# Optimization experiments

Measured on AMD Instinct MI355X. Metric: run time of the kernel, lower is better.

Reference implementation:

```python
import jax, jax.numpy as jnp
import numpy as np

P = 8192      # num_pois
U = 4096      # num_users
E = 4096      # num directed hyperedges
D = 128       # emb_dim
B = 1024      # batch of user indices
T_UP = 1.0    # args.t1
T_GEO = 1.0   # args.t2
T_P2P = 1.0   # args.t3
ALPHA = 0.8   # constant alpha in Geo_ODEFunc


def setup_inputs() -> dict:
    key = jax.random.key(0)
    ks = jax.random.split(key, 13)
    return {
        "poi_emb_weight": jax.random.normal(ks[0], (P + 1, D), jnp.float32) * 0.02,
        "w_gate_geo": jax.random.normal(ks[1], (D, D), jnp.float32) * 0.05,
        "b_gate_geo": jax.random.normal(ks[2], (1, D), jnp.float32) * 0.05,
        "w_gate_seq": jax.random.normal(ks[3], (D, D), jnp.float32) * 0.05,
        "b_gate_seq": jax.random.normal(ks[4], (1, D), jnp.float32) * 0.05,
        "w_gate_col": jax.random.normal(ks[5], (D, D), jnp.float32) * 0.05,
        "b_gate_col": jax.random.normal(ks[6], (1, D), jnp.float32) * 0.05,
        "HG_up": jax.random.uniform(ks[7], (U, P), jnp.float32) * (1.0 / P),
        "HG_pu": jax.random.uniform(ks[8], (P, U), jnp.float32) * (1.0 / U),
        "HG_poi_src": jax.random.uniform(ks[9], (P, E), jnp.float32) * (1.0 / E),
        "HG_poi_tar": jax.random.uniform(ks[10], (E, P), jnp.float32) * (1.0 / P),
        "poi_geo_graph": jax.random.uniform(ks[11], (P, P), jnp.float32) * (1.0 / P),
        "user_idx": jax.random.randint(ks[12], (B,), 0, U, jnp.int32),
    }


def _gate(pe, w, b):
    # pois_embs * sigmoid(pois_embs @ W + b)
    return pe * jax.nn.sigmoid(pe @ w + b)


def reference(poi_emb_weight, w_gate_geo, b_gate_geo, w_gate_seq, b_gate_seq,
              w_gate_col, b_gate_col, HG_up, HG_pu, HG_poi_src, HG_poi_tar,
              poi_geo_graph, user_idx):
    pe = poi_emb_weight[:-1]                      # drop padding row -> [P, D]
    geo_gate = _gate(pe, w_gate_geo, b_gate_geo)
    seq_gate = _gate(pe, w_gate_seq, b_gate_seq)
    col_gate = _gate(pe, w_gate_col, b_gate_col)

    # U2P ODE, single Euler step on t=[0, T_UP]:
    #   f(x) = (HG_pu@HG_up - I)@x + e, e = x0; A@x factored to avoid [P,P].
    x = col_gate
    hg_pois = x + T_UP * (HG_pu @ (HG_up @ x) - x + x)

    # Geo ODE: f(x) = (alpha/2)*G@x - x + e, e = x0, alpha = 0.8.
    g = geo_gate
    geo_pois = g + T_GEO * ((ALPHA / 2.0) * (poi_geo_graph @ g) - g + g)

    # P2P (directed hypergraph) ODE: A = src@tar, f(x) = (A - I)@x + e.
    s = seq_gate
    trans_pois = s + T_P2P * (HG_poi_src @ (HG_poi_tar @ s) - s + s)

    # structural user embeddings, gathered at batch indices
    hg_users = (HG_up @ hg_pois)[user_idx]        # [B, D]
    geo_users = (HG_up @ geo_pois)[user_idx]      # [B, D]

    # [3P + 2B, D]
    return jnp.concatenate([hg_pois, geo_pois, trans_pois, hg_users, geo_users], axis=0)
```

## Files before the change

kernel.cpp:

```cpp
#include <hip/hip_runtime.h>
#include <hip/hip_bf16.h>

#define PP 8192
#define UU 4096
#define EE 4096
#define BB 1024

using f32x4  = __attribute__((ext_vector_type(4))) float;
using u32x4  = __attribute__((ext_vector_type(4))) unsigned int;
using bf16x8 = __attribute__((ext_vector_type(8))) short;
typedef __hip_bfloat16 bf16_t;

__device__ __forceinline__ unsigned cvt2(float a, float b){
  unsigned r;
  asm("v_cvt_pk_bf16_f32 %0, %1, %2" : "=v"(r) : "v"(a), "v"(b));
  return r;
}

__device__ __forceinline__ void gload16(const void* g, void* l){
  __builtin_amdgcn_global_load_lds((const __attribute__((address_space(1))) void*)g,
                                   (__attribute__((address_space(3))) void*)l, 16, 0, 0);
}

struct Job {
  const float*  A;
  const bf16_t* Bt;
  const float*  add;
  const float*  bvec;
  float*        outF;
  bf16_t*       outT;
  int           outTstride;
  float         scale;
  int           K;
  int           nb;
  int           mode;
};

#define ABUF 32768
#define BBUF 16384
#define BOFF 65536

__global__ __launch_bounds__(256, 1) void gemm_big(Job j0, Job j1, Job j2){
  __shared__ char smem[2*ABUF + 3*BBUF];
  int bid = blockIdx.x;
  Job j = j0;
  if (bid >= j.nb){ bid -= j.nb; j = j1; if (bid >= j.nb){ bid -= j.nb; j = j2; } }
  const int K  = j.K;
  const int S  = K >> 8;
  const int T4 = K >> 6;
  const int m0 = bid << 5;
  const int tid = threadIdx.x;
  const int lane = tid & 63;
  const int wid = tid >> 6;
  const int wm = wid >> 1, wk = wid & 1;
  const int s0 = bid & (S - 1);

  const char* Ab = (const char*)j.A;
  const char* Bb = (const char*)j.Bt;

  size_t a_srcb[8]; unsigned a_ldsb[8];
  #pragma unroll
  for (int i = 0; i < 8; ++i){
    int r = wid*8 + i;
    a_srcb[i] = (size_t)(m0 + r)*(size_t)K*4 + (size_t)((unsigned)(lane*16) ^ ((r & 15) << 4));
    a_ldsb[i] = (unsigned)(r * 1024);
  }
  size_t b_srcb[4]; unsigned b_ldsb[4];
  #pragma unroll
  for (int i = 0; i < 4; ++i){
    int L = wid*4 + i;
    int n = L*8 + (lane>>3);
    b_srcb[i] = (size_t)n*(size_t)K*2 + (size_t)(((lane & 7) << 4) ^ ((n & 7) << 4));
    b_ldsb[i] = (unsigned)(BOFF + L * 1024);
  }

  const int arow = wm*16 + (lane & 15);
  const unsigned aswz = (unsigned)((arow & 15) << 4);
  const unsigned kbase = (unsigned)(wk*128 + ((lane>>4) << 5));
  const unsigned ard = (unsigned)(arow*1024) + (kbase ^ aswz);
  unsigned b_rd[8];
  #pragma unroll
  for (int n0 = 0; n0 < 8; ++n0){
    int n = n0*16 + (lane & 15);
    unsigned c = (unsigned)(wk*64 + ((lane>>4) << 4));
    b_rd[n0] = (unsigned)(BOFF + n*128) + (c ^ ((n & 7) << 4));
  }

  const f32x4 fzero = {0.f, 0.f, 0.f, 0.f};
  f32x4 acc[8];
  #pragma unroll
  for (int i = 0; i < 8; ++i) acc[i] = fzero;

  auto STAGE_A = [&](int s){
    char* l = smem + (unsigned)(s & 1) * ABUF;
    size_t ka = (size_t)((unsigned)(s + s0) & (unsigned)(S - 1)) * 1024;
    #pragma unroll
    for (int i = 0; i < 8; ++i) gload16(Ab + a_srcb[i] + ka, l + a_ldsb[i]);
  };
  auto STAGE_B = [&](int lstep){
    char* l = smem + (unsigned)(lstep % 3) * BBUF;
    size_t kb = (size_t)((unsigned)(lstep + 4*s0) & (unsigned)(T4 - 1)) * 128;
    #pragma unroll
    for (int i = 0; i < 4; ++i) gload16(Bb + b_srcb[i] + kb, l + b_ldsb[i]);
  };
  auto COMP = [&](unsigned aoff, unsigned boff){
    unsigned aa = aoff + ard;
    f32x4 a0, a1;
    asm volatile("ds_read_b128 %0, %2\n\tds_read_b128 %1, %3"
                 : "=&v"(a0), "=&v"(a1) : "v"(aa), "v"(aa ^ 16u));
    bf16x8 b0,b1,b2,b3,b4,b5,b6,b7;
    asm volatile("ds_read_b128 %0, %1" : "=v"(b0) : "v"(boff + b_rd[0]));
    asm volatile("ds_read_b128 %0, %1" : "=v"(b1) : "v"(boff + b_rd[1]));
    asm volatile("ds_read_b128 %0, %1" : "=v"(b2) : "v"(boff + b_rd[2]));
    asm volatile("ds_read_b128 %0, %1" : "=v"(b3) : "v"(boff + b_rd[3]));
    asm volatile("ds_read_b128 %0, %1" : "=v"(b4) : "v"(boff + b_rd[4]));
    asm volatile("ds_read_b128 %0, %1" : "=v"(b5) : "v"(boff + b_rd[5]));
    asm volatile("ds_read_b128 %0, %1" : "=v"(b6) : "v"(boff + b_rd[6]));
    asm volatile("ds_read_b128 %0, %1" : "=v"(b7) : "v"(boff + b_rd[7]));
    asm volatile("s_waitcnt lgkmcnt(0)" ::: "memory");
    __builtin_amdgcn_sched_barrier(0);
    union { bf16x8 v; unsigned u[4]; } af;
    af.u[0] = cvt2(a0.x, a0.y);
    af.u[1] = cvt2(a0.z, a0.w);
    af.u[2] = cvt2(a1.x, a1.y);
    af.u[3] = cvt2(a1.z, a1.w);
    acc[0] = __builtin_amdgcn_mfma_f32_16x16x32_bf16(af.v, b0, acc[0], 0,0,0);
    acc[1] = __builtin_amdgcn_mfma_f32_16x16x32_bf16(af.v, b1, acc[1], 0,0,0);
    acc[2] = __builtin_amdgcn_mfma_f32_16x16x32_bf16(af.v, b2, acc[2], 0,0,0);
    acc[3] = __builtin_amdgcn_mfma_f32_16x16x32_bf16(af.v, b3, acc[3], 0,0,0);
    acc[4] = __builtin_amdgcn_mfma_f32_16x16x32_bf16(af.v, b4, acc[4], 0,0,0);
    acc[5] = __builtin_amdgcn_mfma_f32_16x16x32_bf16(af.v, b5, acc[5], 0,0,0);
    acc[6] = __builtin_amdgcn_mfma_f32_16x16x32_bf16(af.v, b6, acc[6], 0,0,0);
    acc[7] = __builtin_amdgcn_mfma_f32_16x16x32_bf16(af.v, b7, acc[7], 0,0,0);
  };

  #define WAITV(n) asm volatile("s_waitcnt vmcnt(" #n ")" ::: "memory")
  #define BAR __builtin_amdgcn_s_barrier()

  STAGE_A(0); STAGE_B(0); STAGE_B(1);

  for (int s = 0; s < S - 1; ++s){
    const unsigned ao = (unsigned)(s & 1) * ABUF;
    const int l = 4*s;
    STAGE_A(s + 1); STAGE_B(l + 2);
    WAITV(16); BAR; COMP(ao + 0*256, (unsigned)((l+0) % 3) * BBUF); BAR;
    STAGE_B(l + 3);
    WAITV(16); BAR; COMP(ao + 1*256, (unsigned)((l+1) % 3) * BBUF); BAR;
    STAGE_B(l + 4);
    WAITV(8);  BAR; COMP(ao + 2*256, (unsigned)((l+2) % 3) * BBUF); BAR;
    STAGE_B(l + 5);
    WAITV(8);  BAR; COMP(ao + 3*256, (unsigned)((l+3) % 3) * BBUF); BAR;
  }
  {
    const int s = S - 1;
    const unsigned ao = (unsigned)(s & 1) * ABUF;
    const int l = 4*s;
    STAGE_B(l + 2);
    WAITV(8); BAR; COMP(ao + 0*256, (unsigned)((l+0) % 3) * BBUF); BAR;
    STAGE_B(l + 3);
    WAITV(8); BAR; COMP(ao + 1*256, (unsigned)((l+1) % 3) * BBUF); BAR;
    WAITV(4); BAR; COMP(ao + 2*256, (unsigned)((l+2) % 3) * BBUF); BAR;
    WAITV(0); BAR; COMP(ao + 3*256, (unsigned)((l+3) % 3) * BBUF); BAR;
  }

  __syncthreads();
  float* red = (float*)smem;
  if (wk == 1){
    #pragma unroll
    for (int n0 = 0; n0 < 8; ++n0)
      #pragma unroll
      for (int q = 0; q < 4; ++q){
        int row = wm*16 + ((lane>>4)<<2) + q;
        int col = n0*16 + (lane & 15);
        red[row*128 + col] = acc[n0][q];
      }
  }
  __syncthreads();
  if (wk == 0){
    #pragma unroll
    for (int n0 = 0; n0 < 8; ++n0)
      #pragma unroll
      for (int q = 0; q < 4; ++q){
        int row = wm*16 + ((lane>>4)<<2) + q;
        int col = n0*16 + (lane & 15);
        float v = (acc[n0][q] + red[row*128 + col]) * j.scale;
        size_t gp = (size_t)(m0 + row);
        if (j.mode == 1){
          float pe = j.add[gp*128 + col];
          float bb = j.bvec[col];
          v = pe / (1.f + __expf(-(v + bb)));
        } else if (j.add){
          v += j.add[gp*128 + col];
        }
        acc[n0][q] = v;
        if (j.outF) j.outF[gp*128 + col] = v;
      }
  }

  if (j.outT){
    __syncthreads();
    if (wk == 0){
      #pragma unroll
      for (int n0 = 0; n0 < 8; ++n0)
        #pragma unroll
        for (int q = 0; q < 4; ++q){
          int row = wm*16 + ((lane>>4)<<2) + q;
          int col = n0*16 + (lane & 15);
          red[row*128 + col] = acc[n0][q];
        }
    }
    __syncthreads();
    int col = tid & 127, seg = tid >> 7;
    unsigned wrds[8] __attribute__((aligned(16)));
    #pragma unroll
    for (int r = 0; r < 8; ++r){
      float v0 = red[(seg*16 + 2*r    )*128 + col];
      float v1 = red[(seg*16 + 2*r + 1)*128 + col];
      wrds[r] = cvt2(v0, v1);
    }
    bf16_t* dst = j.outT + (size_t)col * (size_t)j.outTstride + (m0 + seg*16);
    *(u32x4*)dst       = *(const u32x4*)&wrds[0];
    *((u32x4*)dst + 1) = *(const u32x4*)&wrds[4];
  }
}

#define GTBUF 24576

__global__ __launch_bounds__(256, 2) void gemm_gates(Job j0, Job j1, Job j2){
  __shared__ char smem[3*GTBUF];
  int bid = blockIdx.x;
  Job j = j0;
  if (bid >= j.nb){ bid -= j.nb; j = j1; if (bid >= j.nb){ bid -= j.nb; j = j2; } }
  const int K = j.K;
  const int T = K >> 6;
  const int m0 = bid << 5;
  const int tid = threadIdx.x;
  const int lane = tid & 63;
  const int wid = tid >> 6;
  const int wm = wid >> 1, wk = wid & 1;

  const char* Ab = (const char*)j.A;
  const char* Bb = (const char*)j.Bt;

  size_t a_src[2]; unsigned a_lds[2];
  #pragma unroll
  for (int i = 0; i < 2; ++i){
    int row = wid*8 + i*4 + (lane>>4);
    unsigned sb = (lane & 15) << 4;
    a_src[i] = (size_t)(m0 + row)*(size_t)K*4 + (size_t)(sb ^ ((row & 15) << 4));
    a_lds[i] = (unsigned)((wid*8 + i*4) * 256);
  }
  size_t b_src[4]; unsigned b_lds[4];
  #pragma unroll
  for (int i = 0; i < 4; ++i){
    int n  = wid*32 + i*8 + (lane>>3);
    unsigned sb = (lane & 7) << 4;
    b_src[i] = (size_t)n*(size_t)K*2 + (size_t)(sb ^ ((n & 7) << 4));
    b_lds[i] = (unsigned)(8192 + (wid*32 + i*8) * 128);
  }

  const int arow = wm*16 + (lane & 15);
  const unsigned acb  = (unsigned)(wk*128 + ((lane>>4) * 32));
  const unsigned aswz = (unsigned)((arow & 15) << 4);
  const unsigned a_rd0 = arow*256 + (acb ^ aswz);
  const unsigned a_rd1 = arow*256 + ((acb + 16) ^ aswz);
  unsigned b_rd[8];
  #pragma unroll
  for (int n0 = 0; n0 < 8; ++n0){
    int n = n0*16 + (lane & 15);
    unsigned c = (unsigned)(wk*64 + ((lane>>4) * 16));
    b_rd[n0] = 8192u + n*128 + (c ^ ((n & 7) << 4));
  }

  const f32x4 fzero = {0.f, 0.f, 0.f, 0.f};
  f32x4 acc[8];
  #pragma unroll
  for (int i = 0; i < 8; ++i) acc[i] = fzero;

  auto STAGE = [&](unsigned bufoff, int t){
    char* l = smem + bufoff;
    size_t ka = (size_t)t * 256;
    size_t kb = (size_t)t * 128;
    #pragma unroll
    for (int i = 0; i < 2; ++i) gload16(Ab + a_src[i] + ka, l + a_lds[i]);
    #pragma unroll
    for (int i = 0; i < 4; ++i) gload16(Bb + b_src[i] + kb, l + b_lds[i]);
  };

  STAGE(0, 0);
  if (T > 1){
    STAGE(GTBUF, 1);
    asm volatile("s_waitcnt vmcnt(6)" ::: "memory");
  } else {
    asm volatile("s_waitcnt vmcnt(0)" ::: "memory");
  }
  __builtin_amdgcn_s_barrier();

  for (int t = 0; t < T; ++t){
    char* l = smem + (unsigned)(t % 3) * GTBUF;
    if (t + 2 < T) STAGE((unsigned)((t+2) % 3) * GTBUF, t + 2);
    f32x4 a0 = *(const f32x4*)(l + a_rd0);
    f32x4 a1 = *(const f32x4*)(l + a_rd1);
    union { bf16x8 v; unsigned u[4]; } af;
    af.u[0] = cvt2(a0.x, a0.y);
    af.u[1] = cvt2(a0.z, a0.w);
    af.u[2] = cvt2(a1.x, a1.y);
    af.u[3] = cvt2(a1.z, a1.w);
    #pragma unroll
    for (int n0 = 0; n0 < 8; ++n0){
      bf16x8 bfr = *(const bf16x8*)(l + b_rd[n0]);
      acc[n0] = __builtin_amdgcn_mfma_f32_16x16x32_bf16(af.v, bfr, acc[n0], 0, 0, 0);
    }
    if (t + 1 < T){
      if (t + 2 < T) asm volatile("s_waitcnt vmcnt(6)" ::: "memory");
      else           asm volatile("s_waitcnt vmcnt(0)" ::: "memory");
      __builtin_amdgcn_s_barrier();
    }
  }

  __syncthreads();
  float* red = (float*)smem;
  if (wk == 1){
    #pragma unroll
    for (int n0 = 0; n0 < 8; ++n0)
      #pragma unroll
      for (int q = 0; q < 4; ++q){
        int row = wm*16 + ((lane>>4)<<2) + q;
        int col = n0*16 + (lane & 15);
        red[row*128 + col] = acc[n0][q];
      }
  }
  __syncthreads();
  if (wk == 0){
    #pragma unroll
    for (int n0 = 0; n0 < 8; ++n0)
      #pragma unroll
      for (int q = 0; q < 4; ++q){
        int row = wm*16 + ((lane>>4)<<2) + q;
        int col = n0*16 + (lane & 15);
        float v = (acc[n0][q] + red[row*128 + col]) * j.scale;
        size_t gp = (size_t)(m0 + row);
        if (j.mode == 1){
          float pe = j.add[gp*128 + col];
          float bb = j.bvec[col];
          v = pe / (1.f + __expf(-(v + bb)));
        } else if (j.add){
          v += j.add[gp*128 + col];
        }
        acc[n0][q] = v;
        if (j.outF) j.outF[gp*128 + col] = v;
      }
  }

  if (j.outT){
    __syncthreads();
    if (wk == 0){
      #pragma unroll
      for (int n0 = 0; n0 < 8; ++n0)
        #pragma unroll
        for (int q = 0; q < 4; ++q){
          int row = wm*16 + ((lane>>4)<<2) + q;
          int col = n0*16 + (lane & 15);
          red[row*128 + col] = acc[n0][q];
        }
    }
    __syncthreads();
    int col = tid & 127, seg = tid >> 7;
    unsigned wrds[8] __attribute__((aligned(16)));
    #pragma unroll
    for (int r = 0; r < 8; ++r){
      float v0 = red[(seg*16 + 2*r    )*128 + col];
      float v1 = red[(seg*16 + 2*r + 1)*128 + col];
      wrds[r] = cvt2(v0, v1);
    }
    bf16_t* dst = j.outT + (size_t)col * (size_t)j.outTstride + (m0 + seg*16);
    *(u32x4*)dst       = *(const u32x4*)&wrds[0];
    *((u32x4*)dst + 1) = *(const u32x4*)&wrds[4];
  }
}

#define GBUFB 40960

__global__ __launch_bounds__(256, 1) void gemm_gather(const float* __restrict__ Aup,
    const int* __restrict__ uidx, const bf16_t* __restrict__ B5t, float* __restrict__ partials){
  __shared__ char smem[3*GBUFB];
  const int bid = blockIdx.x;
  const int mtile = bid & 31, split = bid >> 5;
  const int tid = threadIdx.x, lane = tid & 63, wid = tid >> 6;
  const int wm = wid >> 1, wk = wid & 1;
  const int T = 16;
  const char* Ab = (const char*)Aup;
  const char* Bb = (const char*)B5t;

  size_t a_src[2]; unsigned a_lds[2];
  #pragma unroll
  for (int i = 0; i < 2; ++i){
    int row  = wid*8 + i*4 + (lane>>4);
    int grow = uidx[mtile*32 + row];
    unsigned sb = (lane & 15) << 4;
    a_src[i] = (size_t)grow*(size_t)(PP*4) + (size_t)((sb ^ ((row & 15) << 4)) + split*4096);
    a_lds[i] = (unsigned)((wid*8 + i*4) * 256);
  }
  size_t b_src[8]; unsigned b_lds[8];
  #pragma unroll
  for (int i = 0; i < 8; ++i){
    int n  = wid*64 + i*8 + (lane>>3);
    unsigned sb = (lane & 7) << 4;
    b_src[i] = (size_t)n*(size_t)(PP*2) + (size_t)((sb ^ ((n & 7) << 4)) + split*2048);
    b_lds[i] = (unsigned)(8192 + (wid*64 + i*8) * 128);
  }
  const int arow = wm*16 + (lane & 15);
  const unsigned acb  = (unsigned)(wk*128 + ((lane>>4)*32));
  const unsigned aswz = (unsigned)((arow & 15) << 4);
  const unsigned a_rd0 = arow*256 + (acb ^ aswz);
  const unsigned a_rd1 = arow*256 + ((acb + 16) ^ aswz);
  unsigned b_rd[16];
  #pragma unroll
  for (int n0 = 0; n0 < 16; ++n0){
    int n = n0*16 + (lane & 15);
    unsigned c = (unsigned)(wk*64 + ((lane>>4)*16));
    b_rd[n0] = 8192u + n*128 + (c ^ ((n & 7) << 4));
  }
  const f32x4 fzero = {0.f,0.f,0.f,0.f};
  f32x4 acc[16];
  #pragma unroll
  for (int i = 0; i < 16; ++i) acc[i] = fzero;

  auto STAGE = [&](unsigned bufoff, int t){
    char* l = smem + bufoff;
    size_t ka = (size_t)t*256, kb = (size_t)t*128;
    #pragma unroll
    for (int i = 0; i < 2; ++i) gload16(Ab + a_src[i] + ka, l + a_lds[i]);
    #pragma unroll
    for (int i = 0; i < 8; ++i) gload16(Bb + b_src[i] + kb, l + b_lds[i]);
  };
  STAGE(0, 0);
  STAGE(GBUFB, 1);
  asm volatile("s_waitcnt vmcnt(10)" ::: "memory");
  __builtin_amdgcn_s_barrier();
  for (int t = 0; t < T; ++t){
    char* l = smem + (unsigned)(t % 3) * GBUFB;
    if (t + 2 < T) STAGE((unsigned)((t+2)%3)*GBUFB, t+2);
    f32x4 a0 = *(const f32x4*)(l + a_rd0);
    f32x4 a1 = *(const f32x4*)(l + a_rd1);
    union { bf16x8 v; unsigned u[4]; } af;
    af.u[0] = cvt2(a0.x, a0.y);
    af.u[1] = cvt2(a0.z, a0.w);
    af.u[2] = cvt2(a1.x, a1.y);
    af.u[3] = cvt2(a1.z, a1.w);
    #pragma unroll
    for (int n0 = 0; n0 < 16; ++n0){
      bf16x8 bfr = *(const bf16x8*)(l + b_rd[n0]);
      acc[n0] = __builtin_amdgcn_mfma_f32_16x16x32_bf16(af.v, bfr, acc[n0], 0,0,0);
    }
    if (t + 1 < T){
      if (t + 2 < T) asm volatile("s_waitcnt vmcnt(10)" ::: "memory");
      else           asm volatile("s_waitcnt vmcnt(0)" ::: "memory");
      __builtin_amdgcn_s_barrier();
    }
  }
  __syncthreads();
  float* red = (float*)smem;
  if (wk == 1){
    #pragma unroll
    for (int n0 = 0; n0 < 16; ++n0)
      #pragma unroll
      for (int q = 0; q < 4; ++q){
        int row = wm*16 + ((lane>>4)<<2) + q;
        int col = n0*16 + (lane & 15);
        red[row*256 + col] = acc[n0][q];
      }
  }
  __syncthreads();
  if (wk == 0){
    #pragma unroll
    for (int n0 = 0; n0 < 16; ++n0)
      #pragma unroll
      for (int q = 0; q < 4; ++q){
        int row = wm*16 + ((lane>>4)<<2) + q;
        int col = n0*16 + (lane & 15);
        float v = acc[n0][q] + red[row*256 + col];
        partials[((size_t)split*1024 + mtile*32 + row)*256 + col] = v;
      }
  }
}

__global__ void prep_wt(const float* w0, const float* w1, const float* w2,
                        bf16_t* o0, bf16_t* o1, bf16_t* o2){
  const float* w = (blockIdx.x == 0) ? w0 : (blockIdx.x == 1) ? w1 : w2;
  bf16_t*      o = (blockIdx.x == 0) ? o0 : (blockIdx.x == 1) ? o1 : o2;
  int tid = threadIdx.x;
  int n = tid >> 1, h = tid & 1;
  unsigned wr[32] __attribute__((aligned(16)));
  #pragma unroll
  for (int r = 0; r < 32; ++r){
    float v0 = w[(h*64 + 2*r    )*128 + n];
    float v1 = w[(h*64 + 2*r + 1)*128 + n];
    wr[r] = cvt2(v0, v1);
  }
  u32x4* dst = (u32x4*)(o + n*128 + h*64);
  #pragma unroll
  for (int i = 0; i < 8; ++i) dst[i] = *(const u32x4*)&wr[i*4];
}

__global__ void reduce_users(const float* __restrict__ partials, float* __restrict__ out){
  int idx = blockIdx.x * 256 + threadIdx.x;
  int b = idx >> 8, n = idx & 255;
  float s = 0.f;
  #pragma unroll
  for (int k = 0; k < 8; ++k) s += partials[((size_t)k*1024 + b)*256 + n];
  if (n < 128) out[((size_t)(3*PP) + b)*128 + n]           = s;
  else         out[((size_t)(3*PP) + BB + b)*128 + (n-128)] = s;
}

extern "C" void kernel_launch(void* const* d_in, const int* in_sizes, int n_in,
                              void* d_out, int out_size, void* d_ws, size_t ws_size,
                              hipStream_t stream){
  const float* pe   = (const float*)d_in[0];
  const float* wgeo = (const float*)d_in[1];
  const float* bgeo = (const float*)d_in[2];
  const float* wseq = (const float*)d_in[3];
  const float* bseq = (const float*)d_in[4];
  const float* wcol = (const float*)d_in[5];
  const float* bcol = (const float*)d_in[6];
  const float* hup  = (const float*)d_in[7];
  const float* hpu  = (const float*)d_in[8];
  const float* hsrc = (const float*)d_in[9];
  const float* htar = (const float*)d_in[10];
  const float* geo  = (const float*)d_in[11];
  const int*   uidx = (const int*)d_in[12];
  float* out = (float*)d_out;

  char* w = (char*)d_ws;
  const size_t MB = 1024*1024;
  float*  x_f32 = (float*)(w);
  float*  g_f32 = (float*)(w + 4*MB);
  float*  s_f32 = (float*)(w + 8*MB);
  bf16_t* xT    = (bf16_t*)(w + 12*MB);
  bf16_t* gT    = (bf16_t*)(w + 14*MB);
  bf16_t* sT    = (bf16_t*)(w + 16*MB);
  bf16_t* upT   = (bf16_t*)(w + 18*MB);
  bf16_t* tarT  = (bf16_t*)(w + 19*MB);
  bf16_t* b5t   = (bf16_t*)(w + 20*MB);
  bf16_t* wtg   = (bf16_t*)(w + 24*MB);
  bf16_t* wts   = (bf16_t*)(w + 24*MB + 32768);
  bf16_t* wtc   = (bf16_t*)(w + 24*MB + 65536);
  float*  parts = (float*)(w + 25*MB);

  prep_wt<<<3, 256, 0, stream>>>(wgeo, wseq, wcol, wtg, wts, wtc);

  Job jg{pe, wtg, pe, bgeo, g_f32, gT, PP, 1.f, 128, 256, 1};
  Job js{pe, wts, pe, bseq, s_f32, sT, PP, 1.f, 128, 256, 1};
  Job jc{pe, wtc, pe, bcol, x_f32, xT, PP, 1.f, 128, 256, 1};
  gemm_gates<<<768, 256, 0, stream>>>(jg, js, jc);

  Job j1 {hup,  xT, nullptr, nullptr, nullptr,               upT,                  UU, 1.f,  PP, 128, 0};
  Job j3 {geo,  gT, g_f32,   nullptr, out + (size_t)PP*128,  b5t + (size_t)128*PP, PP, 0.4f, PP, 256, 0};
  Job j4a{htar, sT, nullptr, nullptr, nullptr,               tarT,                 EE, 1.f,  PP, 128, 0};
  gemm_big<<<512, 256, 0, stream>>>(j1, j3, j4a);

  Job j2 {hpu,  upT,  x_f32, nullptr, out,                     b5t,     PP, 1.f, UU, 256, 0};
  Job j4b{hsrc, tarT, s_f32, nullptr, out + (size_t)2*PP*128,  nullptr, 0,  1.f, EE, 256, 0};
  Job jd = j4b; jd.nb = 0;
  gemm_big<<<512, 256, 0, stream>>>(j2, j4b, jd);

  gemm_gather<<<256, 256, 0, stream>>>(hup, uidx, b5t, parts);
  reduce_users<<<1024, 256, 0, stream>>>(parts, out);
}
```

Baseline: 313.6 us.

## Replace direct-to-LDS staging with register-staged double-buffered GEMM pipeline

The big GEMM kernel used to stage data with global_load_lds into a 2-deep A buffer and a 3-deep B buffer, about 112KB of LDS. It now loads each 64-wide K tile into registers, writes it to one of two 24KB LDS buffers, and computes on the other. The smaller LDS footprint lets launch bounds allow 2 blocks per CU, which should improve latency hiding and occupancy. In exchange it adds register pressure from the staged tiles, an explicit ds_write pass, and more barriers per K step. It also drops the per-block K rotation that previously spread DRAM accesses across blocks.

```diff
diff --git a/kernel.cpp b/kernel.cpp
--- a/kernel.cpp
+++ b/kernel.cpp
@@ -36,89 +36,93 @@
   int           mode;
 };
 
-#define ABUF 32768
-#define BBUF 16384
-#define BOFF 65536
-
-__global__ __launch_bounds__(256, 1) void gemm_big(Job j0, Job j1, Job j2){
-  __shared__ char smem[2*ABUF + 3*BBUF];
+#define WAITV(n) asm volatile("s_waitcnt vmcnt(" #n ")" ::: "memory")
+#define LGKM0    asm volatile("s_waitcnt lgkmcnt(0)" ::: "memory")
+#define SBAR     __builtin_amdgcn_sched_barrier(0)
+#define BAR      __builtin_amdgcn_s_barrier()
+
+#define RSBUF 24576
+
+__global__ __launch_bounds__(256, 2) void gemm_rs(Job j0, Job j1, Job j2){
+  __shared__ char smem[2*RSBUF];
   int bid = blockIdx.x;
   Job j = j0;
   if (bid >= j.nb){ bid -= j.nb; j = j1; if (bid >= j.nb){ bid -= j.nb; j = j2; } }
-  const int K  = j.K;
-  const int S  = K >> 8;
-  const int T4 = K >> 6;
+  const int K = j.K;
+  const int T = K >> 6;
   const int m0 = bid << 5;
   const int tid = threadIdx.x;
   const int lane = tid & 63;
   const int wid = tid >> 6;
   const int wm = wid >> 1, wk = wid & 1;
-  const int s0 = bid & (S - 1);
-
-  const char* Ab = (const char*)j.A;
-  const char* Bb = (const char*)j.Bt;
-
-  size_t a_srcb[8]; unsigned a_ldsb[8];
-  #pragma unroll
-  for (int i = 0; i < 8; ++i){
-    int r = wid*8 + i;
-    a_srcb[i] = (size_t)(m0 + r)*(size_t)K*4 + (size_t)((unsigned)(lane*16) ^ ((r & 15) << 4));
-    a_ldsb[i] = (unsigned)(r * 1024);
-  }
-  size_t b_srcb[4]; unsigned b_ldsb[4];
-  #pragma unroll
-  for (int i = 0; i < 4; ++i){
-    int L = wid*4 + i;
-    int n = L*8 + (lane>>3);
-    b_srcb[i] = (size_t)n*(size_t)K*2 + (size_t)(((lane & 7) << 4) ^ ((n & 7) << 4));
-    b_ldsb[i] = (unsigned)(BOFF + L * 1024);
-  }
+
+  const int srow = tid >> 3;
+  const int scol = (tid & 7) * 16;
+  const char* ap  = (const char*)j.A  + (size_t)(m0 + srow)*(size_t)K*4 + (unsigned)scol;
+  const char* bq0 = (const char*)j.Bt + (size_t)(srow      )*(size_t)K*2 + (unsigned)scol;
+  const char* bq1 = (const char*)j.Bt + (size_t)(srow +  32)*(size_t)K*2 + (unsigned)scol;
+  const char* bq2 = (const char*)j.Bt + (size_t)(srow +  64)*(size_t)K*2 + (unsigned)scol;
+  const char* bq3 = (const char*)j.Bt + (size_t)(srow +  96)*(size_t)K*2 + (unsigned)scol;
+
+  const unsigned aswzw = (unsigned)((srow & 15) << 4);
+  const unsigned wa0 = (unsigned)(srow*256) + ((unsigned)scol ^ aswzw);
+  const unsigned wa1 = (unsigned)(srow*256) + (((unsigned)scol + 128u) ^ aswzw);
+  const unsigned bswzw = (unsigned)((srow & 7) << 4);
+  const unsigned wb0 = 8192u + (unsigned)(srow*128) + ((unsigned)scol ^ bswzw);
 
   const int arow = wm*16 + (lane & 15);
+  const unsigned acb  = (unsigned)(wk*128 + ((lane>>4) * 32));
   const unsigned aswz = (unsigned)((arow & 15) << 4);
-  const unsigned kbase = (unsigned)(wk*128 + ((lane>>4) << 5));
-  const unsigned ard = (unsigned)(arow*1024) + (kbase ^ aswz);
+  const unsigned a_rd0 = arow*256 + (acb ^ aswz);
+  const unsigned a_rd1 = arow*256 + ((acb + 16) ^ aswz);
   unsigned b_rd[8];
   #pragma unroll
   for (int n0 = 0; n0 < 8; ++n0){
     int n = n0*16 + (lane & 15);
-    unsigned c = (unsigned)(wk*64 + ((lane>>4) << 4));
-    b_rd[n0] = (unsigned)(BOFF + n*128) + (c ^ ((n & 7) << 4));
-  }
-
-  const f32x4 fzero = {0.f, 0.f, 0.f, 0.f};
+    unsigned c = (unsigned)(wk*64 + ((lane>>4) * 16));
+    b_rd[n0] = 8192u + n*128 + (c ^ ((n & 7) << 4));
+  }
+
   f32x4 acc[8];
+  const f32x4 fzero = {0.f,0.f,0.f,0.f};
   #pragma unroll
   for (int i = 0; i < 8; ++i) acc[i] = fzero;
 
-  auto STAGE_A = [&](int s){
-    char* l = smem + (unsigned)(s & 1) * ABUF;
-    size_t ka = (size_t)((unsigned)(s + s0) & (unsigned)(S - 1)) * 1024;
-    #pragma unroll
-    for (int i = 0; i < 8; ++i) gload16(Ab + a_srcb[i] + ka, l + a_ldsb[i]);
-  };
-  auto STAGE_B = [&](int lstep){
-    char* l = smem + (unsigned)(lstep % 3) * BBUF;
-    size_t kb = (size_t)((unsigned)(lstep + 4*s0) & (unsigned)(T4 - 1)) * 128;
-    #pragma unroll
-    for (int i = 0; i < 4; ++i) gload16(Bb + b_srcb[i] + kb, l + b_ldsb[i]);
-  };
-  auto COMP = [&](unsigned aoff, unsigned boff){
-    unsigned aa = aoff + ard;
+  f32x4 eA0,eA1,eB0,eB1,eB2,eB3, oA0,oA1,oB0,oB1,oB2,oB3;
+
+#define RS_ISSUE(A0,A1,B0,B1,B2,B3) do { \
+    asm volatile("global_load_dwordx4 %0, %2, off\n\t" \
+                 "global_load_dwordx4 %1, %2, off offset:128" \
+      : "=&v"(A0), "=&v"(A1) : "v"(ap) : "memory"); \
+    asm volatile("global_load_dwordx4 %0, %1, off" : "=&v"(B0) : "v"(bq0) : "memory"); \
+    asm volatile("global_load_dwordx4 %0, %1, off" : "=&v"(B1) : "v"(bq1) : "memory"); \
+    asm volatile("global_load_dwordx4 %0, %1, off" : "=&v"(B2) : "v"(bq2) : "memory"); \
+    asm volatile("global_load_dwordx4 %0, %1, off" : "=&v"(B3) : "v"(bq3) : "memory"); \
+    ap += 256; bq0 += 128; bq1 += 128; bq2 += 128; bq3 += 128; } while(0)
+
+#define RS_DSW(bo,A0,A1,B0,B1,B2,B3) do { \
+    asm volatile("ds_write_b128 %0, %1" :: "v"((bo) + wa0), "v"(A0) : "memory"); \
+    asm volatile("ds_write_b128 %0, %1" :: "v"((bo) + wa1), "v"(A1) : "memory"); \
+    asm volatile("ds_write_b128 %0, %1"              :: "v"((bo) + wb0), "v"(B0) : "memory"); \
+    asm volatile("ds_write_b128 %0, %1 offset:4096"  :: "v"((bo) + wb0), "v"(B1) : "memory"); \
+    asm volatile("ds_write_b128 %0, %1 offset:8192"  :: "v"((bo) + wb0), "v"(B2) : "memory"); \
+    asm volatile("ds_write_b128 %0, %1 offset:12288" :: "v"((bo) + wb0), "v"(B3) : "memory"); } while(0)
+
+  auto COMP = [&](unsigned bo){
     f32x4 a0, a1;
-    asm volatile("ds_read_b128 %0, %2\n\tds_read_b128 %1, %3"
-                 : "=&v"(a0), "=&v"(a1) : "v"(aa), "v"(aa ^ 16u));
+    asm volatile("ds_read_b128 %0, %1" : "=v"(a0) : "v"(bo + a_rd0));
+    asm volatile("ds_read_b128 %0, %1" : "=v"(a1) : "v"(bo + a_rd1));
     bf16x8 b0,b1,b2,b3,b4,b5,b6,b7;
-    asm volatile("ds_read_b128 %0, %1" : "=v"(b0) : "v"(boff + b_rd[0]));
-    asm volatile("ds_read_b128 %0, %1" : "=v"(b1) : "v"(boff + b_rd[1]));
-    asm volatile("ds_read_b128 %0, %1" : "=v"(b2) : "v"(boff + b_rd[2]));
-    asm volatile("ds_read_b128 %0, %1" : "=v"(b3) : "v"(boff + b_rd[3]));
-    asm volatile("ds_read_b128 %0, %1" : "=v"(b4) : "v"(boff + b_rd[4]));
-    asm volatile("ds_read_b128 %0, %1" : "=v"(b5) : "v"(boff + b_rd[5]));
-    asm volatile("ds_read_b128 %0, %1" : "=v"(b6) : "v"(boff + b_rd[6]));
-    asm volatile("ds_read_b128 %0, %1" : "=v"(b7) : "v"(boff + b_rd[7]));
-    asm volatile("s_waitcnt lgkmcnt(0)" ::: "memory");
-    __builtin_amdgcn_sched_barrier(0);
+    asm volatile("ds_read_b128 %0, %1" : "=v"(b0) : "v"(bo + b_rd[0]));
+    asm volatile("ds_read_b128 %0, %1" : "=v"(b1) : "v"(bo + b_rd[1]));
+    asm volatile("ds_read_b128 %0, %1" : "=v"(b2) : "v"(bo + b_rd[2]));
+    asm volatile("ds_read_b128 %0, %1" : "=v"(b3) : "v"(bo + b_rd[3]));
+    asm volatile("ds_read_b128 %0, %1" : "=v"(b4) : "v"(bo + b_rd[4]));
+    asm volatile("ds_read_b128 %0, %1" : "=v"(b5) : "v"(bo + b_rd[5]));
+    asm volatile("ds_read_b128 %0, %1" : "=v"(b6) : "v"(bo + b_rd[6]));
+    asm volatile("ds_read_b128 %0, %1" : "=v"(b7) : "v"(bo + b_rd[7]));
+    LGKM0;
+    SBAR;
     union { bf16x8 v; unsigned u[4]; } af;
     af.u[0] = cvt2(a0.x, a0.y);
     af.u[1] = cvt2(a0.z, a0.w);
@@ -134,33 +138,25 @@
     acc[7] = __builtin_amdgcn_mfma_f32_16x16x32_bf16(af.v, b7, acc[7], 0,0,0);
   };
 
-  #define WAITV(n) asm volatile("s_waitcnt vmcnt(" #n ")" ::: "memory")
-  #define BAR __builtin_amdgcn_s_barrier()
-
-  STAGE_A(0); STAGE_B(0); STAGE_B(1);
-
-  for (int s = 0; s < S - 1; ++s){
-    const unsigned ao = (unsigned)(s & 1) * ABUF;
-    const int l = 4*s;
-    STAGE_A(s + 1); STAGE_B(l + 2);
-    WAITV(16); BAR; COMP(ao + 0*256, (unsigned)((l+0) % 3) * BBUF); BAR;
-    STAGE_B(l + 3);
-    WAITV(16); BAR; COMP(ao + 1*256, (unsigned)((l+1) % 3) * BBUF); BAR;
-    STAGE_B(l + 4);
-    WAITV(8);  BAR; COMP(ao + 2*256, (unsigned)((l+2) % 3) * BBUF); BAR;
-    STAGE_B(l + 5);
-    WAITV(8);  BAR; COMP(ao + 3*256, (unsigned)((l+3) % 3) * BBUF); BAR;
-  }
-  {
-    const int s = S - 1;
-    const unsigned ao = (unsigned)(s & 1) * ABUF;
-    const int l = 4*s;
-    STAGE_B(l + 2);
-    WAITV(8); BAR; COMP(ao + 0*256, (unsigned)((l+0) % 3) * BBUF); BAR;
-    STAGE_B(l + 3);
-    WAITV(8); BAR; COMP(ao + 1*256, (unsigned)((l+1) % 3) * BBUF); BAR;
-    WAITV(4); BAR; COMP(ao + 2*256, (unsigned)((l+2) % 3) * BBUF); BAR;
-    WAITV(0); BAR; COMP(ao + 3*256, (unsigned)((l+3) % 3) * BBUF); BAR;
+  RS_ISSUE(eA0,eA1,eB0,eB1,eB2,eB3);
+  RS_ISSUE(oA0,oA1,oB0,oB1,oB2,oB3);
+  WAITV(6);
+  RS_DSW(0u, eA0,eA1,eB0,eB1,eB2,eB3);
+  LGKM0; BAR;
+
+  for (int t = 0; t < T; t += 2){
+    if (t + 2 < T) RS_ISSUE(eA0,eA1,eB0,eB1,eB2,eB3);
+    COMP(0u);
+    if (t + 2 < T) WAITV(6); else WAITV(0);
+    RS_DSW(RSBUF, oA0,oA1,oB0,oB1,oB2,oB3);
+    LGKM0; BAR;
+    if (t + 3 < T) RS_ISSUE(oA0,oA1,oB0,oB1,oB2,oB3);
+    COMP(RSBUF);
+    if (t + 2 < T){
+      if (t + 3 < T) WAITV(6); else WAITV(0);
+      RS_DSW(0u, eA0,eA1,eB0,eB1,eB2,eB3);
+      LGKM0; BAR;
+    }
   }
 
   __syncthreads();
@@ -557,12 +553,12 @@
   Job j1 {hup,  xT, nullptr, nullptr, nullptr,               upT,                  UU, 1.f,  PP, 128, 0};
   Job j3 {geo,  gT, g_f32,   nullptr, out + (size_t)PP*128,  b5t + (size_t)128*PP, PP, 0.4f, PP, 256, 0};
   Job j4a{htar, sT, nullptr, nullptr, nullptr,               tarT,                 EE, 1.f,  PP, 128, 0};
-  gemm_big<<<512, 256, 0, stream>>>(j1, j3, j4a);
+  gemm_rs<<<512, 256, 0, stream>>>(j1, j3, j4a);
 
   Job j2 {hpu,  upT,  x_f32, nullptr, out,                     b5t,     PP, 1.f, UU, 256, 0};
   Job j4b{hsrc, tarT, s_f32, nullptr, out + (size_t)2*PP*128,  nullptr, 0,  1.f, EE, 256, 0};
   Job jd = j4b; jd.nb = 0;
-  gemm_big<<<512, 256, 0, stream>>>(j2, j4b, jd);
+  gemm_rs<<<512, 256, 0, stream>>>(j2, j4b, jd);
 
   gemm_gather<<<256, 256, 0, stream>>>(hup, uidx, b5t, parts);
   reduce_users<<<1024, 256, 0, stream>>>(parts, out);
```

Result: faster. 289.7 us (-7.6%).
